# Performance work log

Hardware: AMD Instinct MI355X
Metric: run time of the kernel (lower is better)

The kernel has to match this reference:

```python
import jax, jax.numpy as jnp
import numpy as np
from functools import partial

N = 50000
IN_C, HID_C, OUT_C = 256, 128, 64
E = 800000


def gcn_norm(src, dst, n_nodes):
    # PyG gcn_norm with unit edge weights: deg from target index, D^-1/2 A D^-1/2
    ones = jnp.ones(src.shape[0], dtype=jnp.float32)
    deg = jax.ops.segment_sum(ones, dst, num_segments=n_nodes)
    dinv = jnp.where(deg > 0, jax.lax.rsqrt(deg), 0.0)
    return dinv[src] * dinv[dst]


def gcn_conv(x, src, dst, norm, W, b):
    h = x @ W                              # [N, out] dense GEMM first (PyG order)
    msg = h[src] * norm[:, None]           # gather + scale  [E', out]
    out = jax.ops.segment_sum(msg, dst, num_segments=x.shape[0])
    return out + b


def setup_inputs() -> dict:
    key = jax.random.key(0)
    ks = jax.random.split(key, 6)
    x = jax.random.normal(ks[0], (N, IN_C), dtype=jnp.float32)
    edge_index = jax.random.randint(ks[1], (2, E), 0, N, dtype=jnp.int32)
    # Glorot-ish init for weights
    W1 = jax.random.normal(ks[2], (IN_C, HID_C), dtype=jnp.float32) / np.sqrt(IN_C)
    b1 = jnp.zeros((HID_C,), dtype=jnp.float32)
    W2 = jax.random.normal(ks[3], (HID_C, OUT_C), dtype=jnp.float32) / np.sqrt(HID_C)
    b2 = jnp.zeros((OUT_C,), dtype=jnp.float32)
    return {"x": x, "edge_index": edge_index, "W1": W1, "b1": b1, "W2": W2, "b2": b2}


def reference(x, edge_index, W1, b1, W2, b2):
    # eval mode: dropout is identity
    n = x.shape[0]
    loop = jnp.arange(n, dtype=edge_index.dtype)
    src = jnp.concatenate([edge_index[0], loop])   # add self loops (static E+N)
    dst = jnp.concatenate([edge_index[1], loop])
    norm = gcn_norm(src, dst, n)
    h = jax.nn.relu(gcn_conv(x, src, dst, norm, W1, b1))
    return gcn_conv(h, src, dst, norm, W2, b2)
```

## Files before the change

### kernel.cpp

```cpp
#include <hip/hip_runtime.h>


#define TPB 256
#define NBKT 196
#define EB_CAP 4608
#define CSR_CAP 6400
#define P1_EPB 8192

typedef __bf16 bf16x8 __attribute__((ext_vector_type(8)));
typedef __bf16 bf16x4 __attribute__((ext_vector_type(4)));
typedef __bf16 bf16x2 __attribute__((ext_vector_type(2)));
typedef float f32x4 __attribute__((ext_vector_type(4)));

__device__ __forceinline__ float bflo(unsigned u) { return __uint_as_float(u << 16); }
__device__ __forceinline__ float bfhi(unsigned u) { return __uint_as_float(u & 0xffff0000u); }

__global__ __launch_bounds__(256) void clear_wprep_kernel(
    unsigned* __restrict__ gcnt, float* __restrict__ dinv, __bf16* __restrict__ h2s,
    int N,
    const float* __restrict__ W1, const float* __restrict__ W2,
    __bf16* __restrict__ wf1, __bf16* __restrict__ wf2) {
    if (blockIdx.x == 0) {
        int t = threadIdx.x;
        if (t < NBKT) gcnt[t] = 0;
        if (t == 0) dinv[N] = 0.0f;
        if (t < 32) ((unsigned*)(h2s + (long)N * 64))[t] = 0u;
        return;
    }
    int g = (blockIdx.x - 1) * TPB + threadIdx.x;
    if (g < 64 * 64) {
        int frag = g >> 6, L = g & 63;
        int kstep = frag >> 3, oct = frag & 7;
        int oc = oct * 16 + (L & 15);
        int k0 = kstep * 32 + (L >> 4) * 8;
        bf16x8 v;
#pragma unroll
        for (int j = 0; j < 8; j++) v[j] = (__bf16)W1[(k0 + j) * 128 + oc];
        ((bf16x8*)wf1)[g] = v;
    } else if (g < 64 * 64 + 16 * 64) {
        int g2 = g - 64 * 64;
        int frag = g2 >> 6, L = g2 & 63;
        int kstep = frag >> 2, oct = frag & 3;
        int oc = oct * 16 + (L & 15);
        int k0 = kstep * 32 + (L >> 4) * 8;
        bf16x8 v;
#pragma unroll
        for (int j = 0; j < 8; j++) v[j] = (__bf16)W2[(k0 + j) * 64 + oc];
        ((bf16x8*)wf2)[g2] = v;
    }
}

template <bool IN_BF16, int K, int OC, bool SCALE>
__device__ __forceinline__ void gemm_body(int bid, int tid, const void* __restrict__ Ain,
                                          const bf16x8* __restrict__ wfrag,
                                          const float* __restrict__ dinv,
                                          __bf16* __restrict__ outp, int M) {
    constexpr int KS = K / 32, OT = OC / 16;
    int wave = tid >> 6, lane = tid & 63;
    int col = lane & 15, q = lane >> 4;
    long rb = (long)bid * 128 + wave * 32;
    long r0 = rb + col, r1 = rb + 16 + col;
    long r0c = (r0 < M) ? r0 : (M - 1);
    long r1c = (r1 < M) ? r1 : (M - 1);

    f32x4 acc[OT][2];
#pragma unroll
    for (int o = 0; o < OT; o++) {
        acc[o][0] = (f32x4){0.f, 0.f, 0.f, 0.f};
        acc[o][1] = (f32x4){0.f, 0.f, 0.f, 0.f};
    }

#pragma unroll
    for (int ks = 0; ks < KS; ks++) {
        int k0 = ks * 32 + q * 8;
        bf16x8 b0, b1;
        if constexpr (IN_BF16) {
            const __bf16* A = (const __bf16*)Ain;
            b0 = *(const bf16x8*)(A + r0c * K + k0);
            b1 = *(const bf16x8*)(A + r1c * K + k0);
        } else {
            const float* A = (const float*)Ain;
            float4 f0a = *(const float4*)(A + r0c * K + k0);
            float4 f0b = *(const float4*)(A + r0c * K + k0 + 4);
            float4 f1a = *(const float4*)(A + r1c * K + k0);
            float4 f1b = *(const float4*)(A + r1c * K + k0 + 4);
            b0[0] = (__bf16)f0a.x; b0[1] = (__bf16)f0a.y; b0[2] = (__bf16)f0a.z; b0[3] = (__bf16)f0a.w;
            b0[4] = (__bf16)f0b.x; b0[5] = (__bf16)f0b.y; b0[6] = (__bf16)f0b.z; b0[7] = (__bf16)f0b.w;
            b1[0] = (__bf16)f1a.x; b1[1] = (__bf16)f1a.y; b1[2] = (__bf16)f1a.z; b1[3] = (__bf16)f1a.w;
            b1[4] = (__bf16)f1b.x; b1[5] = (__bf16)f1b.y; b1[6] = (__bf16)f1b.z; b1[7] = (__bf16)f1b.w;
        }
#pragma unroll
        for (int ot = 0; ot < OT; ot++) {
            bf16x8 a = wfrag[(ks * OT + ot) * 64 + lane];
            acc[ot][0] = __builtin_amdgcn_mfma_f32_16x16x32_bf16(a, b0, acc[ot][0], 0, 0, 0);
            acc[ot][1] = __builtin_amdgcn_mfma_f32_16x16x32_bf16(a, b1, acc[ot][1], 0, 0, 0);
        }
    }

    float sc0 = 1.f, sc1 = 1.f;
    if constexpr (SCALE) {
        sc0 = dinv[r0c];
        sc1 = dinv[r1c];
    }
#pragma unroll
    for (int ot = 0; ot < OT; ot++) {
        int oc = ot * 16 + q * 4;
        if (r0 < M) {
            bf16x4 v;
#pragma unroll
            for (int r = 0; r < 4; r++) v[r] = (__bf16)(acc[ot][0][r] * sc0);
            *(bf16x4*)(outp + r0 * OC + oc) = v;
        }
        if (r1 < M) {
            bf16x4 v;
#pragma unroll
            for (int r = 0; r < 4; r++) v[r] = (__bf16)(acc[ot][1][r] * sc1);
            *(bf16x4*)(outp + r1 * OC + oc) = v;
        }
    }
}

__global__ __launch_bounds__(256) void p1_gemm1_kernel(
    const int* __restrict__ src, const int* __restrict__ dst, int E, int p1Blocks,
    unsigned* __restrict__ gcnt, unsigned* __restrict__ ebuf,
    const float* __restrict__ x, const bf16x8* __restrict__ wf1,
    __bf16* __restrict__ h1u, int M) {
    __shared__ unsigned sPacked[P1_EPB];
    __shared__ int sCnt[256];
    if ((int)blockIdx.x < p1Blocks) {
        int t = threadIdx.x;
        sCnt[t] = 0;
        __syncthreads();
        long e0 = (long)blockIdx.x * P1_EPB;
        int cnt = (int)(E - e0);
        if (cnt > P1_EPB) cnt = P1_EPB;
        for (int i = t; i < cnt; i += 256) {
            unsigned s = (unsigned)src[e0 + i];
            unsigned d = (unsigned)dst[e0 + i];
            sPacked[i] = (s << 16) | d;
            atomicAdd(&sCnt[d >> 8], 1);
        }
        __syncthreads();
        int base = 0;
        if (t < NBKT) base = (int)atomicAdd(&gcnt[t], (unsigned)sCnt[t]);
        __syncthreads();
        if (t < NBKT) sCnt[t] = t * EB_CAP + base;
        __syncthreads();
        for (int i = t; i < cnt; i += 256) {
            unsigned p = sPacked[i];
            int b = (int)((p & 0xffffu) >> 8);
            int pos = atomicAdd(&sCnt[b], 1);
            if (pos < (b + 1) * EB_CAP) ebuf[pos] = p;
        }
    } else {
        gemm_body<false, 256, 128, false>(blockIdx.x - p1Blocks, threadIdx.x,
                                          x, wf1, nullptr, h1u, M);
    }
}

__global__ __launch_bounds__(256) void csr_kernel(
    const unsigned* __restrict__ gcnt, const unsigned* __restrict__ ebuf,
    int* __restrict__ csr, int2* __restrict__ se, float* __restrict__ dinv, int N) {
    __shared__ unsigned sEdges[EB_CAP];
    __shared__ int sCnt[256];
    __shared__ int sScan[256];
    int b = blockIdx.x, t = threadIdx.x;
    int m = (int)gcnt[b];
    if (m > EB_CAP) m = EB_CAP;
    sCnt[t] = 0;
    __syncthreads();
    const unsigned* eb = ebuf + b * EB_CAP;
    for (int i = t; i < m; i += 256) {
        unsigned p = eb[i];
        sEdges[i] = p;
        atomicAdd(&sCnt[p & 255u], 1);
    }
    __syncthreads();
    int c = sCnt[t];
    int pad = (c + 7) & ~7;
    sScan[t] = pad;
    __syncthreads();
    for (int off = 1; off < 256; off <<= 1) {
        int v = (t >= off) ? sScan[t - off] : 0;
        __syncthreads();
        sScan[t] += v;
        __syncthreads();
    }
    int start = b * CSR_CAP + sScan[t] - pad;
    int node = (b << 8) + t;
    if (node < N) {
        se[node] = make_int2(start, start + pad);
        dinv[node] = rsqrtf((float)c + 1.0f);
    }
    __syncthreads();
    sCnt[t] = start;
    __syncthreads();
    for (int i = t; i < m; i += 256) {
        unsigned p = sEdges[i];
        int pos = atomicAdd(&sCnt[p & 255u], 1);
        csr[pos] = (int)(p >> 16);
    }
    if (node < N) {
        for (int k = start + c; k < start + pad; k++) csr[k] = N;
    }
}

#define ACC8()                                             \
    do {                                                   \
        a0x += bflo(v0) * w0; a0y += bfhi(v0) * w0;        \
        a1x += bflo(v1) * w1; a1y += bfhi(v1) * w1;        \
        a2x += bflo(v2) * w2; a2y += bfhi(v2) * w2;        \
        a3x += bflo(v3) * w3; a3y += bfhi(v3) * w3;        \
        a0x += bflo(v4) * w4; a0y += bfhi(v4) * w4;        \
        a1x += bflo(v5) * w5; a1y += bfhi(v5) * w5;        \
        a2x += bflo(v6) * w6; a2y += bfhi(v6) * w6;        \
        a3x += bflo(v7) * w7; a3y += bfhi(v7) * w7;        \
    } while (0)

__global__ __launch_bounds__(256) void agg128_gemm2_kernel(
    const __bf16* __restrict__ h, const int* __restrict__ csr,
    const int2* __restrict__ se, const float* __restrict__ dinv,
    const float* __restrict__ bias, const bf16x8* __restrict__ wf2,
    __bf16* __restrict__ h2s, int N) {
    __shared__ __bf16 stash[16 * 132];
    int wave = threadIdx.x >> 6, lane = threadIdx.x & 63;
    int n0 = blockIdx.x * 16;
    unsigned* stw = (unsigned*)stash;

    float2 bv = ((const float2*)bias)[lane];
#pragma unroll 1
    for (int i = 0; i < 4; i++) {
        int n = n0 + wave * 4 + i;
        float ox = 0.f, oy = 0.f;
        if (n < N) {
            int2 s_e = se[n];
            int start = s_e.x, m = s_e.y - s_e.x;
            float dn = dinv[n];
            const unsigned* hp = (const unsigned*)h;
            const int* sl = csr + start;
            unsigned self = hp[(long)n * 64 + lane];
            float a0x = bflo(self) * dn, a0y = bfhi(self) * dn;
            float a1x = 0.f, a1y = 0.f, a2x = 0.f, a2y = 0.f, a3x = 0.f, a3y = 0.f;
            if (m > 0) {
                int4 c0 = *(const int4*)sl;
                int4 c1 = *(const int4*)(sl + 4);
                int i0 = __builtin_amdgcn_readfirstlane(c0.x);
                int i1 = __builtin_amdgcn_readfirstlane(c0.y);
                int i2 = __builtin_amdgcn_readfirstlane(c0.z);
                int i3 = __builtin_amdgcn_readfirstlane(c0.w);
                int i4 = __builtin_amdgcn_readfirstlane(c1.x);
                int i5 = __builtin_amdgcn_readfirstlane(c1.y);
                int i6 = __builtin_amdgcn_readfirstlane(c1.z);
                int i7 = __builtin_amdgcn_readfirstlane(c1.w);
                unsigned v0 = hp[(long)i0 * 64 + lane], v1 = hp[(long)i1 * 64 + lane];
                unsigned v2 = hp[(long)i2 * 64 + lane], v3 = hp[(long)i3 * 64 + lane];
                unsigned v4 = hp[(long)i4 * 64 + lane], v5 = hp[(long)i5 * 64 + lane];
                unsigned v6 = hp[(long)i6 * 64 + lane], v7 = hp[(long)i7 * 64 + lane];
                float w0 = dinv[i0], w1 = dinv[i1], w2 = dinv[i2], w3 = dinv[i3];
                float w4 = dinv[i4], w5 = dinv[i5], w6 = dinv[i6], w7 = dinv[i7];
                int4 d0 = *(const int4*)(sl + 8);
                int4 d1 = *(const int4*)(sl + 12);
                for (int j = 8; j < m; j += 8) {
                    int t0 = __builtin_amdgcn_readfirstlane(d0.x);
                    int t1 = __builtin_amdgcn_readfirstlane(d0.y);
                    int t2 = __builtin_amdgcn_readfirstlane(d0.z);
                    int t3 = __builtin_amdgcn_readfirstlane(d0.w);
                    int t4 = __builtin_amdgcn_readfirstlane(d1.x);
                    int t5 = __builtin_amdgcn_readfirstlane(d1.y);
                    int t6 = __builtin_amdgcn_readfirstlane(d1.z);
                    int t7 = __builtin_amdgcn_readfirstlane(d1.w);
                    unsigned u0 = hp[(long)t0 * 64 + lane], u1 = hp[(long)t1 * 64 + lane];
                    unsigned u2 = hp[(long)t2 * 64 + lane], u3 = hp[(long)t3 * 64 + lane];
                    unsigned u4 = hp[(long)t4 * 64 + lane], u5 = hp[(long)t5 * 64 + lane];
                    unsigned u6 = hp[(long)t6 * 64 + lane], u7 = hp[(long)t7 * 64 + lane];
                    float q0 = dinv[t0], q1 = dinv[t1], q2 = dinv[t2], q3 = dinv[t3];
                    float q4 = dinv[t4], q5 = dinv[t5], q6 = dinv[t6], q7 = dinv[t7];
                    d0 = *(const int4*)(sl + j + 8);
                    d1 = *(const int4*)(sl + j + 12);
                    ACC8();
                    v0 = u0; v1 = u1; v2 = u2; v3 = u3; v4 = u4; v5 = u5; v6 = u6; v7 = u7;
                    w0 = q0; w1 = q1; w2 = q2; w3 = q3; w4 = q4; w5 = q5; w6 = q6; w7 = q7;
                }
                ACC8();
            }
            ox = fmaxf((a0x + a1x + a2x + a3x) * dn + bv.x, 0.f);
            oy = fmaxf((a0y + a1y + a2y + a3y) * dn + bv.y, 0.f);
        }
        bf16x2 st = {(__bf16)ox, (__bf16)oy};
        stw[(wave * 4 + i) * 66 + lane] = *(unsigned*)&st;
    }
    __syncthreads();

    int col = lane & 15, q = lane >> 4;
    const __bf16* srow = stash + col * 132;
    f32x4 acc = (f32x4){0.f, 0.f, 0.f, 0.f};
#pragma unroll
    for (int ks = 0; ks < 4; ks++) {
        bf16x8 bb = *(const bf16x8*)(srow + ks * 32 + q * 8);
        bf16x8 a = wf2[(ks * 4 + wave) * 64 + lane];
        acc = __builtin_amdgcn_mfma_f32_16x16x32_bf16(a, bb, acc, 0, 0, 0);
    }
    int node = n0 + col;
    if (node < N) {
        float dn2 = dinv[node];
        bf16x4 v;
#pragma unroll
        for (int r = 0; r < 4; r++) v[r] = (__bf16)(acc[r] * dn2);
        *(bf16x4*)(h2s + (long)node * 64 + (wave * 16 + q * 4)) = v;
    }
}
#undef ACC8

#define ACC8B()                                                                            \
    do {                                                                                   \
        a0 += __uint_as_float((unsigned)v0 << 16); a1 += __uint_as_float((unsigned)v1 << 16); \
        a2 += __uint_as_float((unsigned)v2 << 16); a3 += __uint_as_float((unsigned)v3 << 16); \
        a0 += __uint_as_float((unsigned)v4 << 16); a1 += __uint_as_float((unsigned)v5 << 16); \
        a2 += __uint_as_float((unsigned)v6 << 16); a3 += __uint_as_float((unsigned)v7 << 16); \
    } while (0)

__global__ __launch_bounds__(256) void agg64_kernel(const __bf16* __restrict__ hs,
                                                    const int* __restrict__ csr,
                                                    const int2* __restrict__ se,
                                                    const float* __restrict__ dinv,
                                                    const float* __restrict__ bias,
                                                    float* __restrict__ outp, int N) {
    int gid = blockIdx.x * TPB + threadIdx.x;
    int n = gid >> 6, lane = gid & 63;
    if (n >= N) return;
    int2 s_e = se[n];
    int start = s_e.x, m = s_e.y - s_e.x;
    float dn = dinv[n];
    const unsigned short* hp = (const unsigned short*)hs;
    const int* sl = csr + start;
    float a0 = __uint_as_float(((unsigned)hp[(long)n * 64 + lane]) << 16);
    float a1 = 0.f, a2 = 0.f, a3 = 0.f;
    if (m > 0) {
        int4 c0 = *(const int4*)sl;
        int4 c1 = *(const int4*)(sl + 4);
        int i0 = __builtin_amdgcn_readfirstlane(c0.x);
        int i1 = __builtin_amdgcn_readfirstlane(c0.y);
        int i2 = __builtin_amdgcn_readfirstlane(c0.z);
        int i3 = __builtin_amdgcn_readfirstlane(c0.w);
        int i4 = __builtin_amdgcn_readfirstlane(c1.x);
        int i5 = __builtin_amdgcn_readfirstlane(c1.y);
        int i6 = __builtin_amdgcn_readfirstlane(c1.z);
        int i7 = __builtin_amdgcn_readfirstlane(c1.w);
        unsigned short v0 = hp[(long)i0 * 64 + lane], v1 = hp[(long)i1 * 64 + lane];
        unsigned short v2 = hp[(long)i2 * 64 + lane], v3 = hp[(long)i3 * 64 + lane];
        unsigned short v4 = hp[(long)i4 * 64 + lane], v5 = hp[(long)i5 * 64 + lane];
        unsigned short v6 = hp[(long)i6 * 64 + lane], v7 = hp[(long)i7 * 64 + lane];
        int4 d0 = *(const int4*)(sl + 8);
        int4 d1 = *(const int4*)(sl + 12);
        for (int j = 8; j < m; j += 8) {
            int t0 = __builtin_amdgcn_readfirstlane(d0.x);
            int t1 = __builtin_amdgcn_readfirstlane(d0.y);
            int t2 = __builtin_amdgcn_readfirstlane(d0.z);
            int t3 = __builtin_amdgcn_readfirstlane(d0.w);
            int t4 = __builtin_amdgcn_readfirstlane(d1.x);
            int t5 = __builtin_amdgcn_readfirstlane(d1.y);
            int t6 = __builtin_amdgcn_readfirstlane(d1.z);
            int t7 = __builtin_amdgcn_readfirstlane(d1.w);
            unsigned short u0 = hp[(long)t0 * 64 + lane], u1 = hp[(long)t1 * 64 + lane];
            unsigned short u2 = hp[(long)t2 * 64 + lane], u3 = hp[(long)t3 * 64 + lane];
            unsigned short u4 = hp[(long)t4 * 64 + lane], u5 = hp[(long)t5 * 64 + lane];
            unsigned short u6 = hp[(long)t6 * 64 + lane], u7 = hp[(long)t7 * 64 + lane];
            d0 = *(const int4*)(sl + j + 8);
            d1 = *(const int4*)(sl + j + 12);
            ACC8B();
            v0 = u0; v1 = u1; v2 = u2; v3 = u3; v4 = u4; v5 = u5; v6 = u6; v7 = u7;
        }
        ACC8B();
    }
    outp[(long)n * 64 + lane] = (a0 + a1 + a2 + a3) * dn + bias[lane];
}
#undef ACC8B

static inline int cdiv(long a, long b) { return (int)((a + b - 1) / b); }

extern "C" void kernel_launch(void* const* d_in, const int* in_sizes, int n_in,
                              void* d_out, int out_size, void* d_ws, size_t ws_size,
                              hipStream_t stream) {
    const float* x  = (const float*)d_in[0];
    const int*   ei = (const int*)d_in[1];
    const float* W1 = (const float*)d_in[2];
    const float* b1 = (const float*)d_in[3];
    const float* W2 = (const float*)d_in[4];
    const float* b2 = (const float*)d_in[5];

    const int IN_C = 256;
    const int N = in_sizes[0] / IN_C;
    const int E = in_sizes[1] / 2;
    const int* src = ei;
    const int* dst = ei + E;

    char* w = (char*)d_ws;
    size_t off = 0;
    auto alloc = [&](size_t bytes) { void* p = w + off; off = (off + bytes + 255) & ~255ull; return p; };
    __bf16*   h1u  = (__bf16*)alloc((size_t)(N + 1) * 128 * 2);
    __bf16*   h2s  = (__bf16*)alloc((size_t)(N + 1) * 64 * 2);
    unsigned* ebuf = (unsigned*)alloc((size_t)NBKT * EB_CAP * 4);
    int*      csr  = (int*)alloc((size_t)NBKT * CSR_CAP * 4);
    int2*     se   = (int2*)alloc((size_t)N * 8);
    float*    dinv = (float*)alloc((size_t)(N + 1) * 4);
    unsigned* gcnt = (unsigned*)alloc(NBKT * 4);
    __bf16*   wf1  = (__bf16*)alloc(64 * 64 * 8 * 2);
    __bf16*   wf2  = (__bf16*)alloc(16 * 64 * 8 * 2);

    int wprepBlocks = cdiv(64 * 64 + 16 * 64, TPB);
    clear_wprep_kernel<<<1 + wprepBlocks, TPB, 0, stream>>>(gcnt, dinv, h2s, N,
                                                            W1, W2, wf1, wf2);

    int p1Blocks = cdiv(E, P1_EPB);
    int gemmBlocks = cdiv(N, 128);
    p1_gemm1_kernel<<<p1Blocks + gemmBlocks, TPB, 0, stream>>>(
        src, dst, E, p1Blocks, gcnt, ebuf, x, (const bf16x8*)wf1, h1u, N);

    csr_kernel<<<NBKT, TPB, 0, stream>>>(gcnt, ebuf, csr, se, dinv, N);

    agg128_gemm2_kernel<<<cdiv(N, 16), TPB, 0, stream>>>(h1u, csr, se, dinv, b1,
                                                         (const bf16x8*)wf2, h2s, N);

    agg64_kernel<<<cdiv((long)N * 64, TPB), TPB, 0, stream>>>(h2s, csr, se, dinv, b2,
                                                              (float*)d_out, N);
}
```

Before: 179.2 us.

## Fuse the four pipeline kernels into one persistent kernel with grid barriers

Merges the edge-bucketing/GEMM1, CSR build, layer-1 aggregation with GEMM2, and layer-2 aggregation kernels into one persistent kernel of 1024 blocks. The phases are separated by software grid barriers built on atomic counters with release and acquire fences. The aim is to remove kernel launch gaps and the tail drain between stages. In exchange, the grid is fixed and blocks loop over virtual blocks. The barrier assumes all 1024 blocks are co-resident and has a bounded spin guard that could break correctness if exceeded.

```diff
diff --git a/kernel.cpp b/kernel.cpp
--- a/kernel.cpp
+++ b/kernel.cpp
@@ -6,6 +6,7 @@
 #define EB_CAP 4608
 #define CSR_CAP 6400
 #define P1_EPB 8192
+#define MEGA_GRID 1024
 
 typedef __bf16 bf16x8 __attribute__((ext_vector_type(8)));
 typedef __bf16 bf16x4 __attribute__((ext_vector_type(4)));
@@ -15,14 +16,30 @@
 __device__ __forceinline__ float bflo(unsigned u) { return __uint_as_float(u << 16); }
 __device__ __forceinline__ float bfhi(unsigned u) { return __uint_as_float(u & 0xffff0000u); }
 
+__device__ __forceinline__ void mega_bar(unsigned* slot, unsigned nblk) {
+    __syncthreads();
+    if (threadIdx.x == 0) {
+        __builtin_amdgcn_fence(__ATOMIC_RELEASE, "agent");
+        __hip_atomic_fetch_add(slot, 1u, __ATOMIC_RELAXED, __HIP_MEMORY_SCOPE_AGENT);
+        int guard = 0;
+        while (__hip_atomic_load(slot, __ATOMIC_RELAXED, __HIP_MEMORY_SCOPE_AGENT) < nblk) {
+            __builtin_amdgcn_s_sleep(8);
+            if (++guard > (1 << 20)) break;
+        }
+        __builtin_amdgcn_fence(__ATOMIC_ACQUIRE, "agent");
+    }
+    __syncthreads();
+}
+
 __global__ __launch_bounds__(256) void clear_wprep_kernel(
     unsigned* __restrict__ gcnt, float* __restrict__ dinv, __bf16* __restrict__ h2s,
-    int N,
+    int N, unsigned* __restrict__ bar,
     const float* __restrict__ W1, const float* __restrict__ W2,
     __bf16* __restrict__ wf1, __bf16* __restrict__ wf2) {
     if (blockIdx.x == 0) {
         int t = threadIdx.x;
         if (t < NBKT) gcnt[t] = 0;
+        if (t < 8) bar[t] = 0u;
         if (t == 0) dinv[N] = 0.0f;
         if (t < 32) ((unsigned*)(h2s + (long)N * 64))[t] = 0u;
         return;
@@ -120,197 +137,6 @@
     }
 }
 
-__global__ __launch_bounds__(256) void p1_gemm1_kernel(
-    const int* __restrict__ src, const int* __restrict__ dst, int E, int p1Blocks,
-    unsigned* __restrict__ gcnt, unsigned* __restrict__ ebuf,
-    const float* __restrict__ x, const bf16x8* __restrict__ wf1,
-    __bf16* __restrict__ h1u, int M) {
-    __shared__ unsigned sPacked[P1_EPB];
-    __shared__ int sCnt[256];
-    if ((int)blockIdx.x < p1Blocks) {
-        int t = threadIdx.x;
-        sCnt[t] = 0;
-        __syncthreads();
-        long e0 = (long)blockIdx.x * P1_EPB;
-        int cnt = (int)(E - e0);
-        if (cnt > P1_EPB) cnt = P1_EPB;
-        for (int i = t; i < cnt; i += 256) {
-            unsigned s = (unsigned)src[e0 + i];
-            unsigned d = (unsigned)dst[e0 + i];
-            sPacked[i] = (s << 16) | d;
-            atomicAdd(&sCnt[d >> 8], 1);
-        }
-        __syncthreads();
-        int base = 0;
-        if (t < NBKT) base = (int)atomicAdd(&gcnt[t], (unsigned)sCnt[t]);
-        __syncthreads();
-        if (t < NBKT) sCnt[t] = t * EB_CAP + base;
-        __syncthreads();
-        for (int i = t; i < cnt; i += 256) {
-            unsigned p = sPacked[i];
-            int b = (int)((p & 0xffffu) >> 8);
-            int pos = atomicAdd(&sCnt[b], 1);
-            if (pos < (b + 1) * EB_CAP) ebuf[pos] = p;
-        }
-    } else {
-        gemm_body<false, 256, 128, false>(blockIdx.x - p1Blocks, threadIdx.x,
-                                          x, wf1, nullptr, h1u, M);
-    }
-}
-
-__global__ __launch_bounds__(256) void csr_kernel(
-    const unsigned* __restrict__ gcnt, const unsigned* __restrict__ ebuf,
-    int* __restrict__ csr, int2* __restrict__ se, float* __restrict__ dinv, int N) {
-    __shared__ unsigned sEdges[EB_CAP];
-    __shared__ int sCnt[256];
-    __shared__ int sScan[256];
-    int b = blockIdx.x, t = threadIdx.x;
-    int m = (int)gcnt[b];
-    if (m > EB_CAP) m = EB_CAP;
-    sCnt[t] = 0;
-    __syncthreads();
-    const unsigned* eb = ebuf + b * EB_CAP;
-    for (int i = t; i < m; i += 256) {
-        unsigned p = eb[i];
-        sEdges[i] = p;
-        atomicAdd(&sCnt[p & 255u], 1);
-    }
-    __syncthreads();
-    int c = sCnt[t];
-    int pad = (c + 7) & ~7;
-    sScan[t] = pad;
-    __syncthreads();
-    for (int off = 1; off < 256; off <<= 1) {
-        int v = (t >= off) ? sScan[t - off] : 0;
-        __syncthreads();
-        sScan[t] += v;
-        __syncthreads();
-    }
-    int start = b * CSR_CAP + sScan[t] - pad;
-    int node = (b << 8) + t;
-    if (node < N) {
-        se[node] = make_int2(start, start + pad);
-        dinv[node] = rsqrtf((float)c + 1.0f);
-    }
-    __syncthreads();
-    sCnt[t] = start;
-    __syncthreads();
-    for (int i = t; i < m; i += 256) {
-        unsigned p = sEdges[i];
-        int pos = atomicAdd(&sCnt[p & 255u], 1);
-        csr[pos] = (int)(p >> 16);
-    }
-    if (node < N) {
-        for (int k = start + c; k < start + pad; k++) csr[k] = N;
-    }
-}
-
-#define ACC8()                                             \
-    do {                                                   \
-        a0x += bflo(v0) * w0; a0y += bfhi(v0) * w0;        \
-        a1x += bflo(v1) * w1; a1y += bfhi(v1) * w1;        \
-        a2x += bflo(v2) * w2; a2y += bfhi(v2) * w2;        \
-        a3x += bflo(v3) * w3; a3y += bfhi(v3) * w3;        \
-        a0x += bflo(v4) * w4; a0y += bfhi(v4) * w4;        \
-        a1x += bflo(v5) * w5; a1y += bfhi(v5) * w5;        \
-        a2x += bflo(v6) * w6; a2y += bfhi(v6) * w6;        \
-        a3x += bflo(v7) * w7; a3y += bfhi(v7) * w7;        \
-    } while (0)
-
-__global__ __launch_bounds__(256) void agg128_gemm2_kernel(
-    const __bf16* __restrict__ h, const int* __restrict__ csr,
-    const int2* __restrict__ se, const float* __restrict__ dinv,
-    const float* __restrict__ bias, const bf16x8* __restrict__ wf2,
-    __bf16* __restrict__ h2s, int N) {
-    __shared__ __bf16 stash[16 * 132];
-    int wave = threadIdx.x >> 6, lane = threadIdx.x & 63;
-    int n0 = blockIdx.x * 16;
-    unsigned* stw = (unsigned*)stash;
-
-    float2 bv = ((const float2*)bias)[lane];
-#pragma unroll 1
-    for (int i = 0; i < 4; i++) {
-        int n = n0 + wave * 4 + i;
-        float ox = 0.f, oy = 0.f;
-        if (n < N) {
-            int2 s_e = se[n];
-            int start = s_e.x, m = s_e.y - s_e.x;
-            float dn = dinv[n];
-            const unsigned* hp = (const unsigned*)h;
-            const int* sl = csr + start;
-            unsigned self = hp[(long)n * 64 + lane];
-            float a0x = bflo(self) * dn, a0y = bfhi(self) * dn;
-            float a1x = 0.f, a1y = 0.f, a2x = 0.f, a2y = 0.f, a3x = 0.f, a3y = 0.f;
-            if (m > 0) {
-                int4 c0 = *(const int4*)sl;
-                int4 c1 = *(const int4*)(sl + 4);
-                int i0 = __builtin_amdgcn_readfirstlane(c0.x);
-                int i1 = __builtin_amdgcn_readfirstlane(c0.y);
-                int i2 = __builtin_amdgcn_readfirstlane(c0.z);
-                int i3 = __builtin_amdgcn_readfirstlane(c0.w);
-                int i4 = __builtin_amdgcn_readfirstlane(c1.x);
-                int i5 = __builtin_amdgcn_readfirstlane(c1.y);
-                int i6 = __builtin_amdgcn_readfirstlane(c1.z);
-                int i7 = __builtin_amdgcn_readfirstlane(c1.w);
-                unsigned v0 = hp[(long)i0 * 64 + lane], v1 = hp[(long)i1 * 64 + lane];
-                unsigned v2 = hp[(long)i2 * 64 + lane], v3 = hp[(long)i3 * 64 + lane];
-                unsigned v4 = hp[(long)i4 * 64 + lane], v5 = hp[(long)i5 * 64 + lane];
-                unsigned v6 = hp[(long)i6 * 64 + lane], v7 = hp[(long)i7 * 64 + lane];
-                float w0 = dinv[i0], w1 = dinv[i1], w2 = dinv[i2], w3 = dinv[i3];
-                float w4 = dinv[i4], w5 = dinv[i5], w6 = dinv[i6], w7 = dinv[i7];
-                int4 d0 = *(const int4*)(sl + 8);
-                int4 d1 = *(const int4*)(sl + 12);
-                for (int j = 8; j < m; j += 8) {
-                    int t0 = __builtin_amdgcn_readfirstlane(d0.x);
-                    int t1 = __builtin_amdgcn_readfirstlane(d0.y);
-                    int t2 = __builtin_amdgcn_readfirstlane(d0.z);
-                    int t3 = __builtin_amdgcn_readfirstlane(d0.w);
-                    int t4 = __builtin_amdgcn_readfirstlane(d1.x);
-                    int t5 = __builtin_amdgcn_readfirstlane(d1.y);
-                    int t6 = __builtin_amdgcn_readfirstlane(d1.z);
-                    int t7 = __builtin_amdgcn_readfirstlane(d1.w);
-                    unsigned u0 = hp[(long)t0 * 64 + lane], u1 = hp[(long)t1 * 64 + lane];
-                    unsigned u2 = hp[(long)t2 * 64 + lane], u3 = hp[(long)t3 * 64 + lane];
-                    unsigned u4 = hp[(long)t4 * 64 + lane], u5 = hp[(long)t5 * 64 + lane];
-                    unsigned u6 = hp[(long)t6 * 64 + lane], u7 = hp[(long)t7 * 64 + lane];
-                    float q0 = dinv[t0], q1 = dinv[t1], q2 = dinv[t2], q3 = dinv[t3];
-                    float q4 = dinv[t4], q5 = dinv[t5], q6 = dinv[t6], q7 = dinv[t7];
-                    d0 = *(const int4*)(sl + j + 8);
-                    d1 = *(const int4*)(sl + j + 12);
-                    ACC8();
-                    v0 = u0; v1 = u1; v2 = u2; v3 = u3; v4 = u4; v5 = u5; v6 = u6; v7 = u7;
-                    w0 = q0; w1 = q1; w2 = q2; w3 = q3; w4 = q4; w5 = q5; w6 = q6; w7 = q7;
-                }
-                ACC8();
-            }
-            ox = fmaxf((a0x + a1x + a2x + a3x) * dn + bv.x, 0.f);
-            oy = fmaxf((a0y + a1y + a2y + a3y) * dn + bv.y, 0.f);
-        }
-        bf16x2 st = {(__bf16)ox, (__bf16)oy};
-        stw[(wave * 4 + i) * 66 + lane] = *(unsigned*)&st;
-    }
-    __syncthreads();
-
-    int col = lane & 15, q = lane >> 4;
-    const __bf16* srow = stash + col * 132;
-    f32x4 acc = (f32x4){0.f, 0.f, 0.f, 0.f};
-#pragma unroll
-    for (int ks = 0; ks < 4; ks++) {
-        bf16x8 bb = *(const bf16x8*)(srow + ks * 32 + q * 8);
-        bf16x8 a = wf2[(ks * 4 + wave) * 64 + lane];
-        acc = __builtin_amdgcn_mfma_f32_16x16x32_bf16(a, bb, acc, 0, 0, 0);
-    }
-    int node = n0 + col;
-    if (node < N) {
-        float dn2 = dinv[node];
-        bf16x4 v;
-#pragma unroll
-        for (int r = 0; r < 4; r++) v[r] = (__bf16)(acc[r] * dn2);
-        *(bf16x4*)(h2s + (long)node * 64 + (wave * 16 + q * 4)) = v;
-    }
-}
-#undef ACC8
-
 #define ACC8B()                                                                            \
     do {                                                                                   \
         a0 += __uint_as_float((unsigned)v0 << 16); a1 += __uint_as_float((unsigned)v1 << 16); \
@@ -319,15 +145,12 @@
         a2 += __uint_as_float((unsigned)v6 << 16); a3 += __uint_as_float((unsigned)v7 << 16); \
     } while (0)
 
-__global__ __launch_bounds__(256) void agg64_kernel(const __bf16* __restrict__ hs,
-                                                    const int* __restrict__ csr,
-                                                    const int2* __restrict__ se,
-                                                    const float* __restrict__ dinv,
-                                                    const float* __restrict__ bias,
-                                                    float* __restrict__ outp, int N) {
-    int gid = blockIdx.x * TPB + threadIdx.x;
-    int n = gid >> 6, lane = gid & 63;
-    if (n >= N) return;
+__device__ __forceinline__ void agg64_node(int n, int lane, const __bf16* __restrict__ hs,
+                                           const int* __restrict__ csr,
+                                           const int2* __restrict__ se,
+                                           const float* __restrict__ dinv,
+                                           const float* __restrict__ bias,
+                                           float* __restrict__ outp) {
     int2 s_e = se[n];
     int start = s_e.x, m = s_e.y - s_e.x;
     float dn = dinv[n];
@@ -376,6 +199,204 @@
 }
 #undef ACC8B
 
+#define ACC8()                                             \
+    do {                                                   \
+        a0x += bflo(v0) * w0; a0y += bfhi(v0) * w0;        \
+        a1x += bflo(v1) * w1; a1y += bfhi(v1) * w1;        \
+        a2x += bflo(v2) * w2; a2y += bfhi(v2) * w2;        \
+        a3x += bflo(v3) * w3; a3y += bfhi(v3) * w3;        \
+        a0x += bflo(v4) * w4; a0y += bfhi(v4) * w4;        \
+        a1x += bflo(v5) * w5; a1y += bfhi(v5) * w5;        \
+        a2x += bflo(v6) * w6; a2y += bfhi(v6) * w6;        \
+        a3x += bflo(v7) * w7; a3y += bfhi(v7) * w7;        \
+    } while (0)
+
+__global__ __launch_bounds__(256, 4) void mega_kernel(
+    const int* __restrict__ src, const int* __restrict__ dst, int E, int p1Blocks,
+    int gemmBlocks, int k3Blocks,
+    unsigned* __restrict__ gcnt, unsigned* __restrict__ ebuf,
+    const float* __restrict__ x, const bf16x8* __restrict__ wf1, __bf16* __restrict__ h1u,
+    int* __restrict__ csr, int2* __restrict__ se, float* __restrict__ dinv,
+    const float* __restrict__ b1, const bf16x8* __restrict__ wf2,
+    __bf16* __restrict__ h2s, const float* __restrict__ b2, float* __restrict__ outp,
+    int N, unsigned* __restrict__ bar) {
+    __shared__ unsigned sBuf[P1_EPB];
+    __shared__ int sCnt[256];
+    __shared__ int sScan[256];
+    int t = threadIdx.x;
+    unsigned nblk = gridDim.x;
+    int wave = t >> 6, lane = t & 63;
+
+    for (int vb = (int)blockIdx.x; vb < p1Blocks + gemmBlocks; vb += (int)nblk) {
+        if (vb < p1Blocks) {
+            sCnt[t] = 0;
+            __syncthreads();
+            long e0 = (long)vb * P1_EPB;
+            int cnt = (int)(E - e0);
+            if (cnt > P1_EPB) cnt = P1_EPB;
+            for (int i = t; i < cnt; i += 256) {
+                unsigned s = (unsigned)src[e0 + i];
+                unsigned d = (unsigned)dst[e0 + i];
+                sBuf[i] = (s << 16) | d;
+                atomicAdd(&sCnt[d >> 8], 1);
+            }
+            __syncthreads();
+            int base = 0;
+            if (t < NBKT) base = (int)atomicAdd(&gcnt[t], (unsigned)sCnt[t]);
+            __syncthreads();
+            if (t < NBKT) sCnt[t] = t * EB_CAP + base;
+            __syncthreads();
+            for (int i = t; i < cnt; i += 256) {
+                unsigned p = sBuf[i];
+                int b = (int)((p & 0xffffu) >> 8);
+                int pos = atomicAdd(&sCnt[b], 1);
+                if (pos < (b + 1) * EB_CAP) ebuf[pos] = p;
+            }
+            __syncthreads();
+        } else {
+            gemm_body<false, 256, 128, false>(vb - p1Blocks, t, x, wf1, nullptr, h1u, N);
+        }
+    }
+    mega_bar(bar + 0, nblk);
+
+    for (int b = (int)blockIdx.x; b < NBKT; b += (int)nblk) {
+        int m = (int)gcnt[b];
+        if (m > EB_CAP) m = EB_CAP;
+        sCnt[t] = 0;
+        __syncthreads();
+        const unsigned* eb = ebuf + b * EB_CAP;
+        for (int i = t; i < m; i += 256) {
+            unsigned p = eb[i];
+            sBuf[i] = p;
+            atomicAdd(&sCnt[p & 255u], 1);
+        }
+        __syncthreads();
+        int c = sCnt[t];
+        int pad = (c + 7) & ~7;
+        sScan[t] = pad;
+        __syncthreads();
+        for (int off2 = 1; off2 < 256; off2 <<= 1) {
+            int v = (t >= off2) ? sScan[t - off2] : 0;
+            __syncthreads();
+            sScan[t] += v;
+            __syncthreads();
+        }
+        int start = b * CSR_CAP + sScan[t] - pad;
+        int node = (b << 8) + t;
+        if (node < N) {
+            se[node] = make_int2(start, start + pad);
+            dinv[node] = rsqrtf((float)c + 1.0f);
+        }
+        __syncthreads();
+        sCnt[t] = start;
+        __syncthreads();
+        for (int i = t; i < m; i += 256) {
+            unsigned p = sBuf[i];
+            int pos = atomicAdd(&sCnt[p & 255u], 1);
+            csr[pos] = (int)(p >> 16);
+        }
+        if (node < N) {
+            for (int k = start + c; k < start + pad; k++) csr[k] = N;
+        }
+        __syncthreads();
+    }
+    mega_bar(bar + 1, nblk);
+
+    {
+        __bf16* stash = (__bf16*)sBuf;
+        unsigned* stw = (unsigned*)sBuf;
+        float2 bv = ((const float2*)b1)[lane];
+        for (int vb = (int)blockIdx.x; vb < k3Blocks; vb += (int)nblk) {
+            int n0 = vb * 16;
+#pragma unroll 1
+            for (int i = 0; i < 4; i++) {
+                int n = n0 + wave * 4 + i;
+                float ox = 0.f, oy = 0.f;
+                if (n < N) {
+                    int2 s_e = se[n];
+                    int start = s_e.x, m = s_e.y - s_e.x;
+                    float dn = dinv[n];
+                    const unsigned* hp = (const unsigned*)h1u;
+                    const int* sl = csr + start;
+                    unsigned self = hp[(long)n * 64 + lane];
+                    float a0x = bflo(self) * dn, a0y = bfhi(self) * dn;
+                    float a1x = 0.f, a1y = 0.f, a2x = 0.f, a2y = 0.f, a3x = 0.f, a3y = 0.f;
+                    if (m > 0) {
+                        int4 c0 = *(const int4*)sl;
+                        int4 c1 = *(const int4*)(sl + 4);
+                        int i0 = __builtin_amdgcn_readfirstlane(c0.x);
+                        int i1 = __builtin_amdgcn_readfirstlane(c0.y);
+                        int i2 = __builtin_amdgcn_readfirstlane(c0.z);
+                        int i3 = __builtin_amdgcn_readfirstlane(c0.w);
+                        int i4 = __builtin_amdgcn_readfirstlane(c1.x);
+                        int i5 = __builtin_amdgcn_readfirstlane(c1.y);
+                        int i6 = __builtin_amdgcn_readfirstlane(c1.z);
+                        int i7 = __builtin_amdgcn_readfirstlane(c1.w);
+                        unsigned v0 = hp[(long)i0 * 64 + lane], v1 = hp[(long)i1 * 64 + lane];
+                        unsigned v2 = hp[(long)i2 * 64 + lane], v3 = hp[(long)i3 * 64 + lane];
+                        unsigned v4 = hp[(long)i4 * 64 + lane], v5 = hp[(long)i5 * 64 + lane];
+                        unsigned v6 = hp[(long)i6 * 64 + lane], v7 = hp[(long)i7 * 64 + lane];
+                        float w0 = dinv[i0], w1 = dinv[i1], w2 = dinv[i2], w3 = dinv[i3];
+                        float w4 = dinv[i4], w5 = dinv[i5], w6 = dinv[i6], w7 = dinv[i7];
+                        int4 d0 = *(const int4*)(sl + 8);
+                        int4 d1 = *(const int4*)(sl + 12);
+                        for (int j = 8; j < m; j += 8) {
+                            int t0 = __builtin_amdgcn_readfirstlane(d0.x);
+                            int t1 = __builtin_amdgcn_readfirstlane(d0.y);
+                            int t2 = __builtin_amdgcn_readfirstlane(d0.z);
+                            int t3 = __builtin_amdgcn_readfirstlane(d0.w);
+                            int t4 = __builtin_amdgcn_readfirstlane(d1.x);
+                            int t5 = __builtin_amdgcn_readfirstlane(d1.y);
+                            int t6 = __builtin_amdgcn_readfirstlane(d1.z);
+                            int t7 = __builtin_amdgcn_readfirstlane(d1.w);
+                            unsigned u0 = hp[(long)t0 * 64 + lane], u1 = hp[(long)t1 * 64 + lane];
+                            unsigned u2 = hp[(long)t2 * 64 + lane], u3 = hp[(long)t3 * 64 + lane];
+                            unsigned u4 = hp[(long)t4 * 64 + lane], u5 = hp[(long)t5 * 64 + lane];
+                            unsigned u6 = hp[(long)t6 * 64 + lane], u7 = hp[(long)t7 * 64 + lane];
+                            float q0 = dinv[t0], q1 = dinv[t1], q2 = dinv[t2], q3 = dinv[t3];
+                            float q4 = dinv[t4], q5 = dinv[t5], q6 = dinv[t6], q7 = dinv[t7];
+                            d0 = *(const int4*)(sl + j + 8);
+                            d1 = *(const int4*)(sl + j + 12);
+                            ACC8();
+                            v0 = u0; v1 = u1; v2 = u2; v3 = u3; v4 = u4; v5 = u5; v6 = u6; v7 = u7;
+                            w0 = q0; w1 = q1; w2 = q2; w3 = q3; w4 = q4; w5 = q5; w6 = q6; w7 = q7;
+                        }
+                        ACC8();
+                    }
+                    ox = fmaxf((a0x + a1x + a2x + a3x) * dn + bv.x, 0.f);
+                    oy = fmaxf((a0y + a1y + a2y + a3y) * dn + bv.y, 0.f);
+                }
+                bf16x2 st = {(__bf16)ox, (__bf16)oy};
+                stw[(wave * 4 + i) * 66 + lane] = *(unsigned*)&st;
+            }
+            __syncthreads();
+            int col = lane & 15, q = lane >> 4;
+            const __bf16* srow = stash + col * 132;
+            f32x4 acc = (f32x4){0.f, 0.f, 0.f, 0.f};
+#pragma unroll
+            for (int ks = 0; ks < 4; ks++) {
+                bf16x8 bb = *(const bf16x8*)(srow + ks * 32 + q * 8);
+                bf16x8 a = wf2[(ks * 4 + wave) * 64 + lane];
+                acc = __builtin_amdgcn_mfma_f32_16x16x32_bf16(a, bb, acc, 0, 0, 0);
+            }
+            int node = n0 + col;
+            if (node < N) {
+                float dn2 = dinv[node];
+                bf16x4 v;
+#pragma unroll
+                for (int r = 0; r < 4; r++) v[r] = (__bf16)(acc[r] * dn2);
+                *(bf16x4*)(h2s + (long)node * 64 + (wave * 16 + q * 4)) = v;
+            }
+            __syncthreads();
+        }
+    }
+    mega_bar(bar + 2, nblk);
+
+    for (int n = (int)blockIdx.x * 4 + wave; n < N; n += (int)nblk * 4)
+        agg64_node(n, lane, h2s, csr, se, dinv, b2, outp);
+}
+#undef ACC8
+
 static inline int cdiv(long a, long b) { return (int)((a + b - 1) / b); }
 
 extern "C" void kernel_launch(void* const* d_in, const int* in_sizes, int n_in,
@@ -404,23 +425,19 @@
     int2*     se   = (int2*)alloc((size_t)N * 8);
     float*    dinv = (float*)alloc((size_t)(N + 1) * 4);
     unsigned* gcnt = (unsigned*)alloc(NBKT * 4);
+    unsigned* bar  = (unsigned*)alloc(256);
     __bf16*   wf1  = (__bf16*)alloc(64 * 64 * 8 * 2);
     __bf16*   wf2  = (__bf16*)alloc(16 * 64 * 8 * 2);
 
     int wprepBlocks = cdiv(64 * 64 + 16 * 64, TPB);
-    clear_wprep_kernel<<<1 + wprepBlocks, TPB, 0, stream>>>(gcnt, dinv, h2s, N,
+    clear_wprep_kernel<<<1 + wprepBlocks, TPB, 0, stream>>>(gcnt, dinv, h2s, N, bar,
                                                             W1, W2, wf1, wf2);
 
     int p1Blocks = cdiv(E, P1_EPB);
     int gemmBlocks = cdiv(N, 128);
-    p1_gemm1_kernel<<<p1Blocks + gemmBlocks, TPB, 0, stream>>>(
-        src, dst, E, p1Blocks, gcnt, ebuf, x, (const bf16x8*)wf1, h1u, N);
-
-    csr_kernel<<<NBKT, TPB, 0, stream>>>(gcnt, ebuf, csr, se, dinv, N);
-
-    agg128_gemm2_kernel<<<cdiv(N, 16), TPB, 0, stream>>>(h1u, csr, se, dinv, b1,
-                                                         (const bf16x8*)wf2, h2s, N);
-
-    agg64_kernel<<<cdiv((long)N * 64, TPB), TPB, 0, stream>>>(h2s, csr, se, dinv, b2,
-                                                              (float*)d_out, N);
-}
+    int k3Blocks = cdiv(N, 16);
+    mega_kernel<<<MEGA_GRID, TPB, 0, stream>>>(
+        src, dst, E, p1Blocks, gemmBlocks, k3Blocks, gcnt, ebuf, x,
+        (const bf16x8*)wf1, h1u, csr, se, dinv, b1, (const bf16x8*)wf2, h2s, b2,
+        (float*)d_out, N, bar);
+}
```

New measurement: 540.3 us. 3.02x slower.

## Drop clear/weight-prep kernel via per-block edge slices and inline weight conversion

Applied to the files above, without the earlier changes.

Removes the initial clear and weight-fragment prep launch. The edge binning pass now writes into fixed per-block, per-bucket slices with local counts, so no global atomic counters need zeroing. The CSR kernel gathers those slices itself and also does the sentinel initialisation. Both GEMMs now read fp32 weights directly with strided loads and convert to bf16 inline, which adds redundant weight traffic and conversion work per block. It also imposes a hard cap of 96 edges per block-bucket slice and fixes the binning grid at 98 blocks; edges beyond the cap are silently dropped.

```diff
diff --git a/kernel.cpp b/kernel.cpp
--- a/kernel.cpp
+++ b/kernel.cpp
@@ -3,6 +3,8 @@
 
 #define TPB 256
 #define NBKT 196
+#define P1_BLKS 98
+#define PB_CAP 96
 #define EB_CAP 4608
 #define CSR_CAP 6400
 #define P1_EPB 8192
@@ -15,47 +17,9 @@
 __device__ __forceinline__ float bflo(unsigned u) { return __uint_as_float(u << 16); }
 __device__ __forceinline__ float bfhi(unsigned u) { return __uint_as_float(u & 0xffff0000u); }
 
-__global__ __launch_bounds__(256) void clear_wprep_kernel(
-    unsigned* __restrict__ gcnt, float* __restrict__ dinv, __bf16* __restrict__ h2s,
-    int N,
-    const float* __restrict__ W1, const float* __restrict__ W2,
-    __bf16* __restrict__ wf1, __bf16* __restrict__ wf2) {
-    if (blockIdx.x == 0) {
-        int t = threadIdx.x;
-        if (t < NBKT) gcnt[t] = 0;
-        if (t == 0) dinv[N] = 0.0f;
-        if (t < 32) ((unsigned*)(h2s + (long)N * 64))[t] = 0u;
-        return;
-    }
-    int g = (blockIdx.x - 1) * TPB + threadIdx.x;
-    if (g < 64 * 64) {
-        int frag = g >> 6, L = g & 63;
-        int kstep = frag >> 3, oct = frag & 7;
-        int oc = oct * 16 + (L & 15);
-        int k0 = kstep * 32 + (L >> 4) * 8;
-        bf16x8 v;
-#pragma unroll
-        for (int j = 0; j < 8; j++) v[j] = (__bf16)W1[(k0 + j) * 128 + oc];
-        ((bf16x8*)wf1)[g] = v;
-    } else if (g < 64 * 64 + 16 * 64) {
-        int g2 = g - 64 * 64;
-        int frag = g2 >> 6, L = g2 & 63;
-        int kstep = frag >> 2, oct = frag & 3;
-        int oc = oct * 16 + (L & 15);
-        int k0 = kstep * 32 + (L >> 4) * 8;
-        bf16x8 v;
-#pragma unroll
-        for (int j = 0; j < 8; j++) v[j] = (__bf16)W2[(k0 + j) * 64 + oc];
-        ((bf16x8*)wf2)[g2] = v;
-    }
-}
-
-template <bool IN_BF16, int K, int OC, bool SCALE>
-__device__ __forceinline__ void gemm_body(int bid, int tid, const void* __restrict__ Ain,
-                                          const bf16x8* __restrict__ wfrag,
-                                          const float* __restrict__ dinv,
-                                          __bf16* __restrict__ outp, int M) {
-    constexpr int KS = K / 32, OT = OC / 16;
+__device__ __forceinline__ void gemm1_body(int bid, int tid, const float* __restrict__ x,
+                                           const float* __restrict__ W1,
+                                           __bf16* __restrict__ outp, int M) {
     int wave = tid >> 6, lane = tid & 63;
     int col = lane & 15, q = lane >> 4;
     long rb = (long)bid * 128 + wave * 32;
@@ -63,119 +27,117 @@
     long r0c = (r0 < M) ? r0 : (M - 1);
     long r1c = (r1 < M) ? r1 : (M - 1);
 
-    f32x4 acc[OT][2];
-#pragma unroll
-    for (int o = 0; o < OT; o++) {
+    f32x4 acc[8][2];
+#pragma unroll
+    for (int o = 0; o < 8; o++) {
         acc[o][0] = (f32x4){0.f, 0.f, 0.f, 0.f};
         acc[o][1] = (f32x4){0.f, 0.f, 0.f, 0.f};
     }
 
 #pragma unroll
-    for (int ks = 0; ks < KS; ks++) {
+    for (int ks = 0; ks < 8; ks++) {
         int k0 = ks * 32 + q * 8;
+        const float* A0 = x + r0c * 256 + k0;
+        const float* A1 = x + r1c * 256 + k0;
+        float4 f0a = *(const float4*)A0;
+        float4 f0b = *(const float4*)(A0 + 4);
+        float4 f1a = *(const float4*)A1;
+        float4 f1b = *(const float4*)(A1 + 4);
         bf16x8 b0, b1;
-        if constexpr (IN_BF16) {
-            const __bf16* A = (const __bf16*)Ain;
-            b0 = *(const bf16x8*)(A + r0c * K + k0);
-            b1 = *(const bf16x8*)(A + r1c * K + k0);
-        } else {
-            const float* A = (const float*)Ain;
-            float4 f0a = *(const float4*)(A + r0c * K + k0);
-            float4 f0b = *(const float4*)(A + r0c * K + k0 + 4);
-            float4 f1a = *(const float4*)(A + r1c * K + k0);
-            float4 f1b = *(const float4*)(A + r1c * K + k0 + 4);
-            b0[0] = (__bf16)f0a.x; b0[1] = (__bf16)f0a.y; b0[2] = (__bf16)f0a.z; b0[3] = (__bf16)f0a.w;
-            b0[4] = (__bf16)f0b.x; b0[5] = (__bf16)f0b.y; b0[6] = (__bf16)f0b.z; b0[7] = (__bf16)f0b.w;
-            b1[0] = (__bf16)f1a.x; b1[1] = (__bf16)f1a.y; b1[2] = (__bf16)f1a.z; b1[3] = (__bf16)f1a.w;
-            b1[4] = (__bf16)f1b.x; b1[5] = (__bf16)f1b.y; b1[6] = (__bf16)f1b.z; b1[7] = (__bf16)f1b.w;
-        }
-#pragma unroll
-        for (int ot = 0; ot < OT; ot++) {
-            bf16x8 a = wfrag[(ks * OT + ot) * 64 + lane];
+        b0[0] = (__bf16)f0a.x; b0[1] = (__bf16)f0a.y; b0[2] = (__bf16)f0a.z; b0[3] = (__bf16)f0a.w;
+        b0[4] = (__bf16)f0b.x; b0[5] = (__bf16)f0b.y; b0[6] = (__bf16)f0b.z; b0[7] = (__bf16)f0b.w;
+        b1[0] = (__bf16)f1a.x; b1[1] = (__bf16)f1a.y; b1[2] = (__bf16)f1a.z; b1[3] = (__bf16)f1a.w;
+        b1[4] = (__bf16)f1b.x; b1[5] = (__bf16)f1b.y; b1[6] = (__bf16)f1b.z; b1[7] = (__bf16)f1b.w;
+        const float* wp = W1 + (long)k0 * 128 + col;
+#pragma unroll
+        for (int ot = 0; ot < 8; ot++) {
+            bf16x8 a;
+#pragma unroll
+            for (int j = 0; j < 8; j++) a[j] = (__bf16)wp[j * 128 + ot * 16];
             acc[ot][0] = __builtin_amdgcn_mfma_f32_16x16x32_bf16(a, b0, acc[ot][0], 0, 0, 0);
             acc[ot][1] = __builtin_amdgcn_mfma_f32_16x16x32_bf16(a, b1, acc[ot][1], 0, 0, 0);
         }
     }
 
-    float sc0 = 1.f, sc1 = 1.f;
-    if constexpr (SCALE) {
-        sc0 = dinv[r0c];
-        sc1 = dinv[r1c];
-    }
-#pragma unroll
-    for (int ot = 0; ot < OT; ot++) {
+#pragma unroll
+    for (int ot = 0; ot < 8; ot++) {
         int oc = ot * 16 + q * 4;
         if (r0 < M) {
             bf16x4 v;
 #pragma unroll
-            for (int r = 0; r < 4; r++) v[r] = (__bf16)(acc[ot][0][r] * sc0);
-            *(bf16x4*)(outp + r0 * OC + oc) = v;
+            for (int r = 0; r < 4; r++) v[r] = (__bf16)acc[ot][0][r];
+            *(bf16x4*)(outp + r0 * 128 + oc) = v;
         }
         if (r1 < M) {
             bf16x4 v;
 #pragma unroll
-            for (int r = 0; r < 4; r++) v[r] = (__bf16)(acc[ot][1][r] * sc1);
-            *(bf16x4*)(outp + r1 * OC + oc) = v;
+            for (int r = 0; r < 4; r++) v[r] = (__bf16)acc[ot][1][r];
+            *(bf16x4*)(outp + r1 * 128 + oc) = v;
         }
     }
 }
 
 __global__ __launch_bounds__(256) void p1_gemm1_kernel(
     const int* __restrict__ src, const int* __restrict__ dst, int E, int p1Blocks,
-    unsigned* __restrict__ gcnt, unsigned* __restrict__ ebuf,
-    const float* __restrict__ x, const bf16x8* __restrict__ wf1,
+    unsigned* __restrict__ gcnt2, unsigned* __restrict__ ebuf2,
+    const float* __restrict__ x, const float* __restrict__ W1,
     __bf16* __restrict__ h1u, int M) {
-    __shared__ unsigned sPacked[P1_EPB];
     __shared__ int sCnt[256];
-    if ((int)blockIdx.x < p1Blocks) {
-        int t = threadIdx.x;
+    int bx = (int)blockIdx.x, t = threadIdx.x;
+    if (bx < p1Blocks) {
         sCnt[t] = 0;
         __syncthreads();
-        long e0 = (long)blockIdx.x * P1_EPB;
+        long e0 = (long)bx * P1_EPB;
         int cnt = (int)(E - e0);
         if (cnt > P1_EPB) cnt = P1_EPB;
+        unsigned* myslice = ebuf2 + (long)bx * NBKT * PB_CAP;
         for (int i = t; i < cnt; i += 256) {
             unsigned s = (unsigned)src[e0 + i];
             unsigned d = (unsigned)dst[e0 + i];
-            sPacked[i] = (s << 16) | d;
-            atomicAdd(&sCnt[d >> 8], 1);
+            int b = (int)(d >> 8);
+            int pos = atomicAdd(&sCnt[b], 1);
+            if (pos < PB_CAP) myslice[b * PB_CAP + pos] = (s << 16) | d;
         }
         __syncthreads();
-        int base = 0;
-        if (t < NBKT) base = (int)atomicAdd(&gcnt[t], (unsigned)sCnt[t]);
-        __syncthreads();
-        if (t < NBKT) sCnt[t] = t * EB_CAP + base;
-        __syncthreads();
-        for (int i = t; i < cnt; i += 256) {
-            unsigned p = sPacked[i];
-            int b = (int)((p & 0xffffu) >> 8);
-            int pos = atomicAdd(&sCnt[b], 1);
-            if (pos < (b + 1) * EB_CAP) ebuf[pos] = p;
+        if (t < NBKT) {
+            int c = sCnt[t];
+            gcnt2[bx * NBKT + t] = (unsigned)(c < PB_CAP ? c : PB_CAP);
         }
     } else {
-        gemm_body<false, 256, 128, false>(blockIdx.x - p1Blocks, threadIdx.x,
-                                          x, wf1, nullptr, h1u, M);
+        gemm1_body(bx - p1Blocks, t, x, W1, h1u, M);
     }
 }
 
 __global__ __launch_bounds__(256) void csr_kernel(
-    const unsigned* __restrict__ gcnt, const unsigned* __restrict__ ebuf,
-    int* __restrict__ csr, int2* __restrict__ se, float* __restrict__ dinv, int N) {
+    const unsigned* __restrict__ gcnt2, const unsigned* __restrict__ ebuf2,
+    int* __restrict__ csr, int2* __restrict__ se, float* __restrict__ dinv,
+    __bf16* __restrict__ h2s, int N) {
     __shared__ unsigned sEdges[EB_CAP];
     __shared__ int sCnt[256];
     __shared__ int sScan[256];
+    __shared__ int sTot;
     int b = blockIdx.x, t = threadIdx.x;
-    int m = (int)gcnt[b];
+    if (b == 0) {
+        if (t == 0) dinv[N] = 0.0f;
+        if (t < 32) ((unsigned*)(h2s + (long)N * 64))[t] = 0u;
+    }
+    sCnt[t] = 0;
+    if (t == 0) sTot = 0;
+    __syncthreads();
+    if (t < P1_BLKS) {
+        int c = (int)gcnt2[t * NBKT + b];
+        int pos = atomicAdd(&sTot, c);
+        const unsigned* chunk = ebuf2 + ((long)t * NBKT + b) * PB_CAP;
+        for (int i = 0; i < c; i++) {
+            if (pos + i >= EB_CAP) break;
+            unsigned p = chunk[i];
+            sEdges[pos + i] = p;
+            atomicAdd(&sCnt[p & 255u], 1);
+        }
+    }
+    __syncthreads();
+    int m = sTot;
     if (m > EB_CAP) m = EB_CAP;
-    sCnt[t] = 0;
-    __syncthreads();
-    const unsigned* eb = ebuf + b * EB_CAP;
-    for (int i = t; i < m; i += 256) {
-        unsigned p = eb[i];
-        sEdges[i] = p;
-        atomicAdd(&sCnt[p & 255u], 1);
-    }
-    __syncthreads();
     int c = sCnt[t];
     int pad = (c + 7) & ~7;
     sScan[t] = pad;
@@ -220,7 +182,7 @@
 __global__ __launch_bounds__(256) void agg128_gemm2_kernel(
     const __bf16* __restrict__ h, const int* __restrict__ csr,
     const int2* __restrict__ se, const float* __restrict__ dinv,
-    const float* __restrict__ bias, const bf16x8* __restrict__ wf2,
+    const float* __restrict__ bias, const float* __restrict__ W2,
     __bf16* __restrict__ h2s, int N) {
     __shared__ __bf16 stash[16 * 132];
     int wave = threadIdx.x >> 6, lane = threadIdx.x & 63;
@@ -297,7 +259,10 @@
 #pragma unroll
     for (int ks = 0; ks < 4; ks++) {
         bf16x8 bb = *(const bf16x8*)(srow + ks * 32 + q * 8);
-        bf16x8 a = wf2[(ks * 4 + wave) * 64 + lane];
+        const float* wp = W2 + (long)(ks * 32 + q * 8) * 64 + wave * 16 + col;
+        bf16x8 a;
+#pragma unroll
+        for (int j = 0; j < 8; j++) a[j] = (__bf16)wp[j * 64];
         acc = __builtin_amdgcn_mfma_f32_16x16x32_bf16(a, bb, acc, 0, 0, 0);
     }
     int node = n0 + col;
@@ -397,29 +362,23 @@
     char* w = (char*)d_ws;
     size_t off = 0;
     auto alloc = [&](size_t bytes) { void* p = w + off; off = (off + bytes + 255) & ~255ull; return p; };
-    __bf16*   h1u  = (__bf16*)alloc((size_t)(N + 1) * 128 * 2);
-    __bf16*   h2s  = (__bf16*)alloc((size_t)(N + 1) * 64 * 2);
-    unsigned* ebuf = (unsigned*)alloc((size_t)NBKT * EB_CAP * 4);
-    int*      csr  = (int*)alloc((size_t)NBKT * CSR_CAP * 4);
-    int2*     se   = (int2*)alloc((size_t)N * 8);
-    float*    dinv = (float*)alloc((size_t)(N + 1) * 4);
-    unsigned* gcnt = (unsigned*)alloc(NBKT * 4);
-    __bf16*   wf1  = (__bf16*)alloc(64 * 64 * 8 * 2);
-    __bf16*   wf2  = (__bf16*)alloc(16 * 64 * 8 * 2);
-
-    int wprepBlocks = cdiv(64 * 64 + 16 * 64, TPB);
-    clear_wprep_kernel<<<1 + wprepBlocks, TPB, 0, stream>>>(gcnt, dinv, h2s, N,
-                                                            W1, W2, wf1, wf2);
-
-    int p1Blocks = cdiv(E, P1_EPB);
+    __bf16*   h1u   = (__bf16*)alloc((size_t)(N + 1) * 128 * 2);
+    __bf16*   h2s   = (__bf16*)alloc((size_t)(N + 1) * 64 * 2);
+    unsigned* ebuf2 = (unsigned*)alloc((size_t)P1_BLKS * NBKT * PB_CAP * 4);
+    int*      csr   = (int*)alloc((size_t)NBKT * CSR_CAP * 4);
+    int2*     se    = (int2*)alloc((size_t)N * 8);
+    float*    dinv  = (float*)alloc((size_t)(N + 1) * 4);
+    unsigned* gcnt2 = (unsigned*)alloc((size_t)P1_BLKS * NBKT * 4);
+
+    int p1Blocks = P1_BLKS;
     int gemmBlocks = cdiv(N, 128);
     p1_gemm1_kernel<<<p1Blocks + gemmBlocks, TPB, 0, stream>>>(
-        src, dst, E, p1Blocks, gcnt, ebuf, x, (const bf16x8*)wf1, h1u, N);
-
-    csr_kernel<<<NBKT, TPB, 0, stream>>>(gcnt, ebuf, csr, se, dinv, N);
+        src, dst, E, p1Blocks, gcnt2, ebuf2, x, W1, h1u, N);
+
+    csr_kernel<<<NBKT, TPB, 0, stream>>>(gcnt2, ebuf2, csr, se, dinv, h2s, N);
 
     agg128_gemm2_kernel<<<cdiv(N, 16), TPB, 0, stream>>>(h1u, csr, se, dinv, b1,
-                                                         (const bf16x8*)wf2, h2s, N);
+                                                         W2, h2s, N);
 
     agg64_kernel<<<cdiv((long)N * 64, TPB), TPB, 0, stream>>>(h2s, csr, se, dinv, b2,
                                                               (float*)d_out, N);
```

Measured after the change: 193.2 us. 7.8% more time.
